# Performance work log

Measured on AMD Instinct MI355X. Metric: run time of the kernel, lower is better.

## Reference

```python
import jax, jax.numpy as jnp
import numpy as np

N_ATOMS = 500_000
N_EDGES = 1_000_000
N_BLOCKS = 100_000
HIDDEN = 128
ATOM_VOCAB = 128
BOND_VOCAB = 5


def setup_inputs() -> dict:
    key = jax.random.key(0)
    ks = jax.random.split(key, 12)
    A = jax.random.randint(ks[0], (N_ATOMS,), 0, ATOM_VOCAB)
    src = jax.random.randint(ks[1], (N_EDGES,), 0, N_ATOMS)
    dst = jax.random.randint(ks[2], (N_EDGES,), 0, N_ATOMS)
    btype = jax.random.randint(ks[3], (N_EDGES,), 0, BOND_VOCAB)
    bonds = jnp.stack([src, dst, btype], axis=1)  # [E, 3]
    # monotone atom -> block assignment (like length_to_batch_id)
    block_ids = jnp.sort(jax.random.randint(ks[4], (N_ATOMS,), 0, N_BLOCKS))
    generate_mask = jax.random.bernoulli(ks[5], 0.5, (N_BLOCKS,))
    s = 0.02
    atom_table = jax.random.normal(ks[6], (ATOM_VOCAB, HIDDEN), jnp.float32) * s
    bond_table = jax.random.normal(ks[7], (BOND_VOCAB, HIDDEN), jnp.float32) * s
    eps = jnp.zeros((), jnp.float32)  # GINE epsilon
    W1 = jax.random.normal(ks[8], (HIDDEN, HIDDEN), jnp.float32) * s
    b1 = jnp.zeros((HIDDEN,), jnp.float32)
    W2 = jax.random.normal(ks[9], (HIDDEN, HIDDEN), jnp.float32) * s
    b2 = jnp.zeros((HIDDEN,), jnp.float32)
    return {"A": A, "bonds": bonds, "block_ids": block_ids,
            "generate_mask": generate_mask, "atom_table": atom_table,
            "bond_table": bond_table, "eps": eps,
            "W1": W1, "b1": b1, "W2": W2, "b2": b2}


def reference(A, bonds, block_ids, generate_mask, atom_table, bond_table,
              eps, W1, b1, W2, b2):
    n_atoms = A.shape[0]
    n_blocks = generate_mask.shape[0]
    # context mask per atom; edges kept only if both endpoints are context
    ctx = ~generate_mask[block_ids]                      # [N] bool
    src, dst, btype = bonds[:, 0], bonds[:, 1], bonds[:, 2]
    edge_keep = (ctx[src] & ctx[dst]).astype(atom_table.dtype)[:, None]  # [E,1]
    # embedding gathers
    H = atom_table[A]                                    # [N, D]
    e_attr = bond_table[btype]                           # [E, D]
    # GINEConv: h_i' = MLP((1+eps)*h_i + sum_{j->i} relu(h_j + e_ji))
    # masked edges contribute zero (equivalent to filtering them out)
    msg = jax.nn.relu(H[src] + e_attr) * edge_keep       # [E, D]
    agg = jax.ops.segment_sum(msg, dst, num_segments=n_atoms)  # [N, D]
    h = (1.0 + eps) * H + agg
    h = jax.nn.relu(h @ W1 + b1) @ W2 + b2               # [N, D]
    # std-conserving scatter mean over blocks: sum / sqrt(count)
    blk_sum = jax.ops.segment_sum(h, block_ids, num_segments=n_blocks)  # [B, D]
    cnt = jax.ops.segment_sum(jnp.ones((n_atoms,), h.dtype), block_ids,
                              num_segments=n_blocks)     # [B]
    topo = blk_sum / jnp.sqrt(jnp.maximum(cnt, 1.0))[:, None]
    # zero out the generated (masked) blocks
    topo = jnp.where(generate_mask[:, None], jnp.zeros_like(topo), topo)
    return topo
```

## Files before the change

### kernel.cpp

```cpp
#include <hip/hip_runtime.h>
#include <math.h>

#define NA 500000
#define NE 1000000
#define NB 100000
#define HID 128
#define NCHUNK 489
#define NT 7813
#define NBT 1563
#define NAC 272000
#define CAPA 14
#define SST 132
#define HSB 136
#define NEB 977
#define NAB 1954

typedef __attribute__((ext_vector_type(8))) short bf16x8;
typedef __attribute__((ext_vector_type(4))) float f32x4;

static __device__ __forceinline__ unsigned short bf1(float a) {
    unsigned ua = __float_as_uint(a);
    ua += 0x7fffu + ((ua >> 16) & 1u);
    return (unsigned short)(ua >> 16);
}
static __device__ __forceinline__ unsigned bfpack(float a, float b) {
    unsigned ua = __float_as_uint(a); ua += 0x7fffu + ((ua >> 16) & 1u);
    unsigned ub = __float_as_uint(b); ub += 0x7fffu + ((ub >> 16) & 1u);
    return (ua >> 16) | (ub & 0xffff0000u);
}
static __device__ __forceinline__ float bff(unsigned short h) {
    return __uint_as_float((unsigned)h << 16);
}

__global__ __launch_bounds__(256) void k_scanprep(
    const int* __restrict__ block_ids, const int* __restrict__ gmask,
    const int* __restrict__ A,
    int* __restrict__ cnt, int* __restrict__ acp, int* __restrict__ totB,
    const float* __restrict__ at, const float* __restrict__ bt,
    const float* __restrict__ W1, const float* __restrict__ W2,
    const float* __restrict__ b1, const float* __restrict__ epsp,
    float* __restrict__ TAW, float* __restrict__ MTW,
    unsigned short* __restrict__ wt2)
{
    __shared__ float smem[17920];
    const int blk = blockIdx.x;
    const int tid = threadIdx.x;

    if (blk < NCHUNK) {
        int* sd = (int*)smem;
        int base = blk * 1024 + tid * 4;
        int c0 = 0, c1 = 0, c2 = 0, c3 = 0;
        int4 av = make_int4(0, 0, 0, 0);
        if (base < NA) {
            int4 b = *(const int4*)(block_ids + base);
            av = *(const int4*)(A + base);
            atomicAdd(&cnt[b.x], 1); atomicAdd(&cnt[b.y], 1);
            atomicAdd(&cnt[b.z], 1); atomicAdd(&cnt[b.w], 1);
            c0 = (gmask[b.x] == 0); c1 = (gmask[b.y] == 0);
            c2 = (gmask[b.z] == 0); c3 = (gmask[b.w] == 0);
        }
        int s = c0 + c1 + c2 + c3;
        sd[tid] = s;
        __syncthreads();
        for (int o = 1; o < 256; o <<= 1) {
            int x = (tid >= o) ? sd[tid - o] : 0;
            __syncthreads();
            sd[tid] += x;
            __syncthreads();
        }
        int run = sd[tid] - s;
        if (tid == 255) totB[blk] = sd[255];
        if (base < NA) {
            acp[base + 0] = c0 ? ((run << 7) | av.x) : -1; run += c0;
            acp[base + 1] = c1 ? ((run << 7) | av.y) : -1; run += c1;
            acp[base + 2] = c2 ? ((run << 7) | av.z) : -1; run += c2;
            acp[base + 3] = c3 ? ((run << 7) | av.w) : -1;
        }
    } else if (blk < NCHUNK + 64) {
        const int blk2 = blk - NCHUNK;
        float* sW1 = smem;
        float (*sIn)[HID] = (float(*)[HID])(smem + 16384);
        for (int i = tid; i < HID * HID / 4; i += 256)
            ((float4*)sW1)[i] = ((const float4*)W1)[i];
        for (int x = tid; x < 12 * HID; x += 256) {
            int rr = x >> 7, k = x & 127;
            int r = blk2 * 12 + rr;
            float v = 0.f;
            if (r < 128) v = at[r * HID + k];
            else {
                int m = r - 128;
                int a = m / 5, bb = m - a * 5;
                v = fmaxf(at[a * HID + k] + bt[bb * HID + k], 0.f);
            }
            sIn[rr][k] = v;
        }
        __syncthreads();
        float ope = 1.0f + epsp[0];
        for (int x = tid; x < 12 * HID; x += 256) {
            int rr = x >> 7, c = x & 127;
            int r = blk2 * 12 + rr;
            float acc = 0.f;
#pragma unroll 8
            for (int k = 0; k < HID; ++k)
                acc = fmaf(sIn[rr][k], sW1[k * HID + c], acc);
            if (r < 128) TAW[r * HID + c] = ope * acc + b1[c];
            else         MTW[(r - 128) * HID + c] = acc;
        }
    } else {
        int id = (blk - NCHUNK - 64) * 256 + tid;
        int n = id >> 7, k = id & 127;
        wt2[id] = bf1(W2[k * HID + n]);
    }
}

__global__ __launch_bounds__(256) void k_escfat(
    const int* __restrict__ bonds, const int* __restrict__ acp,
    const int* __restrict__ totB, const int* __restrict__ block_ids,
    int* __restrict__ adeg, unsigned short* __restrict__ buf2,
    int* __restrict__ catomA, int* __restrict__ nctxp,
    float* __restrict__ out)
{
    __shared__ int sT[512];
    __shared__ int sS[256];
    const int t = threadIdx.x;
    int a0 = (2 * t     < NCHUNK) ? totB[2 * t]     : 0;
    int a1 = (2 * t + 1 < NCHUNK) ? totB[2 * t + 1] : 0;
    int s = a0 + a1;
    sS[t] = s;
    __syncthreads();
    for (int o = 1; o < 256; o <<= 1) {
        int x = (t >= o) ? sS[t - o] : 0;
        __syncthreads();
        sS[t] += x;
        __syncthreads();
    }
    int run = sS[t] - s;
    sT[2 * t] = run;
    sT[2 * t + 1] = run + a0;
    if (blockIdx.x == 0 && t == 255) nctxp[0] = sS[255];
    __syncthreads();

    if (blockIdx.x < NEB) {
        int e4 = blockIdx.x * 256 + t;
        if (e4 >= NE / 4) return;
        const int4* b4 = (const int4*)bonds;
        int4 q0 = b4[e4 * 3 + 0];
        int4 q1 = b4[e4 * 3 + 1];
        int4 q2 = b4[e4 * 3 + 2];
        int ss[4] = {q0.x, q0.w, q1.z, q2.y};
        int dd[4] = {q0.y, q1.x, q1.w, q2.z};
        int tt[4] = {q0.z, q1.y, q2.x, q2.w};
#pragma unroll
        for (int k = 0; k < 4; ++k) {
            int va = acp[ss[k]];
            int vd = acp[dd[k]];
            if ((va | vd) >= 0) {
                int pd = (vd >> 7) + sT[dd[k] >> 10];
                int slot = atomicAdd(&adeg[pd], 1);
                if (slot < CAPA)
                    buf2[(size_t)pd * CAPA + slot] =
                        (unsigned short)((va & 127) * 5 + tt[k]);
            }
        }
    } else {
        int i = (blockIdx.x - NEB) * 256 + t;
        if (i < NA) {
            int v = acp[i];
            if (v >= 0) {
                int p = (v >> 7) + sT[i >> 10];
                int bid = block_ids[i];
                catomA[p] = (bid << 7) | (v & 127);
                int pm = p & 31;
                if (pm == 0 || pm == 31) {
                    float4 z = make_float4(0.f, 0.f, 0.f, 0.f);
                    float4* o = (float4*)(out + (size_t)bid * HID);
#pragma unroll
                    for (int j = 0; j < 32; ++j) o[j] = z;
                }
            }
        }
    }
}

__global__ __launch_bounds__(256, 8) void k_h1(
    const int* __restrict__ catomA, const int* __restrict__ nctxp,
    const int* __restrict__ adeg, const unsigned short* __restrict__ buf2,
    const float* __restrict__ TAW, const float* __restrict__ MTW,
    float* __restrict__ out)
{
    __shared__ unsigned short sH[64 * HSB];
    __shared__ int sAid[64];
    __shared__ int sBid[64];
    __shared__ int sDeg[64];

    const int nctx = nctxp[0];
    const int base = blockIdx.x * 64;
    if (base >= nctx) return;
    const int tid = threadIdx.x;

    if (tid < 64) {
        int idx = base + tid;
        if (idx < nctx) {
            int ca = catomA[idx];
            sAid[tid] = ca & 127;
            sBid[tid] = ca >> 7;
            int d = adeg[idx];
            sDeg[tid] = d < CAPA ? d : CAPA;
        } else {
            sAid[tid] = -1; sBid[tid] = -1; sDeg[tid] = 0;
        }
    }
    __syncthreads();

    {
        const int al = tid >> 2;
        const int ks = (tid & 3) * 32;
        const int aid = (base + tid / 4 < nctx) ? sAid[al] : -1;
        float hacc[32];
#pragma unroll
        for (int j = 0; j < 32; ++j) hacc[j] = 0.f;
        if (aid >= 0) {
            const int deg = sDeg[al];
            const unsigned* ep32 = (const unsigned*)(buf2 + (size_t)(base + al) * CAPA);
            unsigned ev[7];
#pragma unroll
            for (int j = 0; j < 7; ++j)
                if (2 * j < deg) ev[j] = ep32[j];
            const float4* tp = (const float4*)(TAW + aid * HID + ks);
#pragma unroll
            for (int j = 0; j < 8; ++j) {
                float4 v = tp[j];
                hacc[4 * j + 0] = v.x; hacc[4 * j + 1] = v.y;
                hacc[4 * j + 2] = v.z; hacc[4 * j + 3] = v.w;
            }
#pragma unroll
            for (int j = 0; j < 7; ++j) {
                if (2 * j < deg) {
                    const float4* mp = (const float4*)(MTW + (int)(ev[j] & 0xffffu) * HID + ks);
#pragma unroll
                    for (int q = 0; q < 8; ++q) {
                        float4 x = mp[q];
                        hacc[4 * q + 0] += x.x; hacc[4 * q + 1] += x.y;
                        hacc[4 * q + 2] += x.z; hacc[4 * q + 3] += x.w;
                    }
                }
                if (2 * j + 1 < deg) {
                    const float4* mp = (const float4*)(MTW + (int)(ev[j] >> 16) * HID + ks);
#pragma unroll
                    for (int q = 0; q < 8; ++q) {
                        float4 x = mp[q];
                        hacc[4 * q + 0] += x.x; hacc[4 * q + 1] += x.y;
                        hacc[4 * q + 2] += x.z; hacc[4 * q + 3] += x.w;
                    }
                }
            }
        }
        unsigned short* rp = sH + al * HSB + ks;
#pragma unroll
        for (int j = 0; j < 4; ++j) {
            uint4 u;
            u.x = bfpack(fmaxf(hacc[8 * j + 0], 0.f), fmaxf(hacc[8 * j + 1], 0.f));
            u.y = bfpack(fmaxf(hacc[8 * j + 2], 0.f), fmaxf(hacc[8 * j + 3], 0.f));
            u.z = bfpack(fmaxf(hacc[8 * j + 4], 0.f), fmaxf(hacc[8 * j + 5], 0.f));
            u.w = bfpack(fmaxf(hacc[8 * j + 6], 0.f), fmaxf(hacc[8 * j + 7], 0.f));
            *(uint4*)(rp + 8 * j) = u;
        }
    }
    __syncthreads();

    {
        int c = tid & 127;
        int r0 = (tid >> 7) * 32;
        float run = 0.f;
        int curb = sBid[r0];
        bool unsafe = (r0 == 0) ? true : (sBid[31] == curb);
        for (int r = r0; r < r0 + 32; ++r) {
            int b = sBid[r];
            if (b != curb) {
                if (curb >= 0) {
                    float* o = out + (size_t)curb * HID + c;
                    if (unsafe) atomicAdd(o, run); else *o = run;
                }
                run = 0.f; curb = b; unsafe = false;
            }
            run += bff(sH[r * HSB + c]);
        }
        if (curb >= 0) {
            bool endUnsafe = (r0 == 0) ? (sBid[32] == curb) : true;
            float* o = out + (size_t)curb * HID + c;
            if (unsafe || endUnsafe) atomicAdd(o, run); else *o = run;
        }
    }
}

__global__ __launch_bounds__(256, 4) void k_gemm2(
    const unsigned short* __restrict__ wt2, const float* __restrict__ b2,
    const int* __restrict__ cnt, const int* __restrict__ gmask,
    float* __restrict__ out)
{
    __shared__ char lds[64 * SST * 4];
    __shared__ float sCnt[64];
    __shared__ float sScale[64];
    const int base = blockIdx.x * 64;
    const int tid = threadIdx.x;

    if (tid < 64) {
        int rb = base + tid;
        float cf = 0.f, sc = 0.f;
        if (rb < NB) {
            int c = cnt[rb];
            cf = (float)c;
            sc = (gmask[rb] == 0) ? rsqrtf((float)(c < 1 ? 1 : c)) : 0.f;
        }
        sCnt[tid] = cf;
        sScale[tid] = sc;
    }

    {
        const int al = tid >> 2;
        const int ks4 = tid & 3;
        const int rb = base + al;
        float v[32];
        if (rb < NB && gmask[rb] == 0 && cnt[rb] > 0) {
            const float4* sp = (const float4*)(out + (size_t)rb * HID + ks4 * 32);
#pragma unroll
            for (int j = 0; j < 8; ++j) {
                float4 x = sp[j];
                v[4 * j + 0] = x.x; v[4 * j + 1] = x.y;
                v[4 * j + 2] = x.z; v[4 * j + 3] = x.w;
            }
        } else {
#pragma unroll
            for (int j = 0; j < 32; ++j) v[j] = 0.f;
        }
        char* rowp = lds + al * 256;
#pragma unroll
        for (int c = 0; c < 4; ++c) {
            uint4 u;
            u.x = bfpack(v[8 * c + 0], v[8 * c + 1]);
            u.y = bfpack(v[8 * c + 2], v[8 * c + 3]);
            u.z = bfpack(v[8 * c + 4], v[8 * c + 5]);
            u.w = bfpack(v[8 * c + 6], v[8 * c + 7]);
            int chunk = (ks4 * 4 + c) ^ (al & 7);
            *(uint4*)(rowp + chunk * 16) = u;
        }
    }
    __syncthreads();

    const int w = tid >> 6;
    const int lane = tid & 63;
    const int rA = w * 16 + (lane & 15);
    const int g4 = lane >> 4;
    const int colb = lane & 15;

    f32x4 acc[8];
    {
        bf16x8 af[4];
#pragma unroll
        for (int k4 = 0; k4 < 4; ++k4) {
            int chunk = (k4 * 4 + g4) ^ (rA & 7);
            af[k4] = *(const bf16x8*)(lds + rA * 256 + chunk * 16);
        }
#pragma unroll
        for (int ct = 0; ct < 8; ++ct) {
            f32x4 a = {0.f, 0.f, 0.f, 0.f};
            const unsigned short* wp = wt2 + (ct * 16 + colb) * HID + g4 * 8;
#pragma unroll
            for (int k4 = 0; k4 < 4; ++k4) {
                bf16x8 bfr = *(const bf16x8*)(wp + k4 * 32);
                a = __builtin_amdgcn_mfma_f32_16x16x32_bf16(af[k4], bfr, a, 0, 0, 0);
            }
            acc[ct] = a;
        }
    }
    __syncthreads();

    float* sF = (float*)lds;
#pragma unroll
    for (int ct = 0; ct < 8; ++ct) {
        int col = ct * 16 + colb;
        float bv = b2[col];
#pragma unroll
        for (int r = 0; r < 4; ++r) {
            int row = w * 16 + g4 * 4 + r;
            sF[row * SST + col] = (acc[ct][r] + sCnt[row] * bv) * sScale[row];
        }
    }
    __syncthreads();

    {
        const int al = tid >> 2;
        const int ks = (tid & 3) * 32;
        const int rb = base + al;
        if (rb < NB) {
            float4* o = (float4*)(out + (size_t)rb * HID + ks);
            const float* rp = sF + al * SST + ks;
#pragma unroll
            for (int j = 0; j < 8; ++j) o[j] = *(const float4*)(rp + 4 * j);
        }
    }
}

extern "C" void kernel_launch(void* const* d_in, const int* in_sizes, int n_in,
                              void* d_out, int out_size, void* d_ws, size_t ws_size,
                              hipStream_t stream) {
    const int* A          = (const int*)d_in[0];
    const int* bonds      = (const int*)d_in[1];
    const int* block_ids  = (const int*)d_in[2];
    const int* gmask      = (const int*)d_in[3];
    const float* atom_table = (const float*)d_in[4];
    const float* bond_table = (const float*)d_in[5];
    const float* eps      = (const float*)d_in[6];
    const float* W1       = (const float*)d_in[7];
    const float* b1       = (const float*)d_in[8];
    const float* W2       = (const float*)d_in[9];
    const float* b2       = (const float*)d_in[10];
    float* out = (float*)d_out;
    char* ws = (char*)d_ws;

    int* cnt    = (int*)(ws + 0);
    int* adeg   = (int*)(ws + 400000);
    int* totB   = (int*)(ws + 1488000);
    int* nctx   = (int*)(ws + 1490000);
    float* TAW  = (float*)(ws + 1490048);
    float* MTW  = (float*)(ws + 1555584);
    unsigned short* wt2 = (unsigned short*)(ws + 1883264);
    int* acp    = (int*)(ws + 1916032);
    int* catomA = (int*)(ws + 3916032);
    unsigned short* buf2 = (unsigned short*)(ws + 5004032);

    hipMemsetAsync(cnt, 0, 1488000, stream);

    k_scanprep<<<NCHUNK + 128, 256, 0, stream>>>(
        block_ids, gmask, A, cnt, acp, totB,
        atom_table, bond_table, W1, W2, b1, eps, TAW, MTW, wt2);
    k_escfat<<<NEB + NAB, 256, 0, stream>>>(
        bonds, acp, totB, block_ids, adeg, buf2, catomA, nctx, out);
    k_h1<<<NT, 256, 0, stream>>>(catomA, nctx, adeg, buf2, TAW, MTW, out);
    k_gemm2<<<NBT, 256, 0, stream>>>(wt2, b2, cnt, gmask, out);
}
```

Measured before the change: 151.0 us.

## Double k_h1 threads per block, swizzle LDS tile, and split reduction into 16-row groups

k_h1 now runs 512 threads per block, with each thread accumulating 16 hidden columns of an atom instead of 32. This halves per-thread registers and doubles the number of outstanding gathers from the TAW/MTW tables. The padded shared-memory tile is replaced by an XOR-swizzled 128-wide layout to avoid bank conflicts without padding. The per-block segment sum now uses four 16-row groups with values preloaded into registers, and the output-zeroing condition in k_escfat is changed to match the new 16-row group boundaries. More group boundaries mean more atomics and more zero-initialisation writes.

```diff
diff --git a/kernel.cpp b/kernel.cpp
--- a/kernel.cpp
+++ b/kernel.cpp
@@ -11,7 +11,6 @@
 #define NAC 272000
 #define CAPA 14
 #define SST 132
-#define HSB 136
 #define NEB 977
 #define NAB 1954
 
@@ -170,8 +169,8 @@
                 int p = (v >> 7) + sT[i >> 10];
                 int bid = block_ids[i];
                 catomA[p] = (bid << 7) | (v & 127);
-                int pm = p & 31;
-                if (pm == 0 || pm == 31) {
+                int pm = p & 15;
+                if (pm == 0 || pm == 15) {
                     float4 z = make_float4(0.f, 0.f, 0.f, 0.f);
                     float4* o = (float4*)(out + (size_t)bid * HID);
 #pragma unroll
@@ -182,13 +181,13 @@
     }
 }
 
-__global__ __launch_bounds__(256, 8) void k_h1(
+__global__ __launch_bounds__(512, 8) void k_h1(
     const int* __restrict__ catomA, const int* __restrict__ nctxp,
     const int* __restrict__ adeg, const unsigned short* __restrict__ buf2,
     const float* __restrict__ TAW, const float* __restrict__ MTW,
     float* __restrict__ out)
 {
-    __shared__ unsigned short sH[64 * HSB];
+    __shared__ unsigned short sH[64 * 128];
     __shared__ int sAid[64];
     __shared__ int sBid[64];
     __shared__ int sDeg[64];
@@ -213,12 +212,12 @@
     __syncthreads();
 
     {
-        const int al = tid >> 2;
-        const int ks = (tid & 3) * 32;
-        const int aid = (base + tid / 4 < nctx) ? sAid[al] : -1;
-        float hacc[32];
-#pragma unroll
-        for (int j = 0; j < 32; ++j) hacc[j] = 0.f;
+        const int al = tid >> 3;
+        const int ks8 = (tid & 7) * 16;
+        const int aid = sAid[al];
+        float hacc[16];
+#pragma unroll
+        for (int j = 0; j < 16; ++j) hacc[j] = 0.f;
         if (aid >= 0) {
             const int deg = sDeg[al];
             const unsigned* ep32 = (const unsigned*)(buf2 + (size_t)(base + al) * CAPA);
@@ -226,9 +225,9 @@
 #pragma unroll
             for (int j = 0; j < 7; ++j)
                 if (2 * j < deg) ev[j] = ep32[j];
-            const float4* tp = (const float4*)(TAW + aid * HID + ks);
-#pragma unroll
-            for (int j = 0; j < 8; ++j) {
+            const float4* tp = (const float4*)(TAW + aid * HID + ks8);
+#pragma unroll
+            for (int j = 0; j < 4; ++j) {
                 float4 v = tp[j];
                 hacc[4 * j + 0] = v.x; hacc[4 * j + 1] = v.y;
                 hacc[4 * j + 2] = v.z; hacc[4 * j + 3] = v.w;
@@ -236,18 +235,18 @@
 #pragma unroll
             for (int j = 0; j < 7; ++j) {
                 if (2 * j < deg) {
-                    const float4* mp = (const float4*)(MTW + (int)(ev[j] & 0xffffu) * HID + ks);
-#pragma unroll
-                    for (int q = 0; q < 8; ++q) {
+                    const float4* mp = (const float4*)(MTW + (int)(ev[j] & 0xffffu) * HID + ks8);
+#pragma unroll
+                    for (int q = 0; q < 4; ++q) {
                         float4 x = mp[q];
                         hacc[4 * q + 0] += x.x; hacc[4 * q + 1] += x.y;
                         hacc[4 * q + 2] += x.z; hacc[4 * q + 3] += x.w;
                     }
                 }
                 if (2 * j + 1 < deg) {
-                    const float4* mp = (const float4*)(MTW + (int)(ev[j] >> 16) * HID + ks);
-#pragma unroll
-                    for (int q = 0; q < 8; ++q) {
+                    const float4* mp = (const float4*)(MTW + (int)(ev[j] >> 16) * HID + ks8);
+#pragma unroll
+                    for (int q = 0; q < 4; ++q) {
                         float4 x = mp[q];
                         hacc[4 * q + 0] += x.x; hacc[4 * q + 1] += x.y;
                         hacc[4 * q + 2] += x.z; hacc[4 * q + 3] += x.w;
@@ -255,27 +254,40 @@
                 }
             }
         }
-        unsigned short* rp = sH + al * HSB + ks;
-#pragma unroll
-        for (int j = 0; j < 4; ++j) {
+        unsigned short* rowbase = sH + al * 128;
+#pragma unroll
+        for (int j = 0; j < 2; ++j) {
+            int pc = ((ks8 >> 3) + j) ^ (al & 7);
             uint4 u;
             u.x = bfpack(fmaxf(hacc[8 * j + 0], 0.f), fmaxf(hacc[8 * j + 1], 0.f));
             u.y = bfpack(fmaxf(hacc[8 * j + 2], 0.f), fmaxf(hacc[8 * j + 3], 0.f));
             u.z = bfpack(fmaxf(hacc[8 * j + 4], 0.f), fmaxf(hacc[8 * j + 5], 0.f));
             u.w = bfpack(fmaxf(hacc[8 * j + 6], 0.f), fmaxf(hacc[8 * j + 7], 0.f));
-            *(uint4*)(rp + 8 * j) = u;
+            *(uint4*)(rowbase + pc * 8) = u;
         }
     }
     __syncthreads();
 
     {
-        int c = tid & 127;
-        int r0 = (tid >> 7) * 32;
+        const int c = tid & 127;
+        const int q = tid >> 7;
+        const int r0 = q * 16;
+        float vals[16];
+        int bids[16];
+#pragma unroll
+        for (int k = 0; k < 16; ++k) {
+            int r = r0 + k;
+            vals[k] = bff(sH[r * 128 + ((((c >> 3) ^ (r & 7)) << 3) | (c & 7))]);
+            bids[k] = sBid[r];
+        }
+        int prev = (q == 0) ? -2 : sBid[r0 - 1];
+        int nxt  = (q == 3) ? -2 : sBid[r0 + 16];
         float run = 0.f;
-        int curb = sBid[r0];
-        bool unsafe = (r0 == 0) ? true : (sBid[31] == curb);
-        for (int r = r0; r < r0 + 32; ++r) {
-            int b = sBid[r];
+        int curb = bids[0];
+        bool unsafe = (q == 0) || (prev == curb);
+#pragma unroll
+        for (int k = 0; k < 16; ++k) {
+            int b = bids[k];
             if (b != curb) {
                 if (curb >= 0) {
                     float* o = out + (size_t)curb * HID + c;
@@ -283,10 +295,10 @@
                 }
                 run = 0.f; curb = b; unsafe = false;
             }
-            run += bff(sH[r * HSB + c]);
+            run += vals[k];
         }
         if (curb >= 0) {
-            bool endUnsafe = (r0 == 0) ? (sBid[32] == curb) : true;
+            bool endUnsafe = (q == 3) || (nxt == curb);
             float* o = out + (size_t)curb * HID + c;
             if (unsafe || endUnsafe) atomicAdd(o, run); else *o = run;
         }
@@ -436,6 +448,6 @@
         atom_table, bond_table, W1, W2, b1, eps, TAW, MTW, wt2);
     k_escfat<<<NEB + NAB, 256, 0, stream>>>(
         bonds, acp, totB, block_ids, adeg, buf2, catomA, nctx, out);
-    k_h1<<<NT, 256, 0, stream>>>(catomA, nctx, adeg, buf2, TAW, MTW, out);
+    k_h1<<<NT, 512, 0, stream>>>(catomA, nctx, adeg, buf2, TAW, MTW, out);
     k_gemm2<<<NBT, 256, 0, stream>>>(wt2, b2, cnt, gmask, out);
 }
```

Result: faster. 136.6 us (-9.6%).
